# Kernel tuning notes

Measured on AMD Instinct MI355X. Metric: run time of the kernel, lower is better.

## Reference

```python
import jax, jax.numpy as jnp
import numpy as np

FR = 44100          # frame_rate
L = 882000          # sound length (20 s @ 44.1 kHz)
T = 2048            # number of onset time steps
H_GRU = 3
H_LSTM = 10


def setup_inputs() -> dict:
    key = jax.random.key(0)
    ks = jax.random.split(key, 20)

    def unif(k, shape, fan):
        b = 1.0 / np.sqrt(fan)
        return jax.random.uniform(k, shape, jnp.float32, -b, b)

    return {
        "sound": jax.random.normal(ks[0], (1, L), jnp.float32),
        "alpha": jnp.sort(jax.random.randint(ks[1], (1, T), 0, L), axis=1),
        # GRU (input_size=FR, hidden=3): gates ordered (r, z, n). W_hh is
        # multiplied by h0=0 (seq_len==1), so only its bias b_hh matters.
        "gru_w_ih": unif(ks[2], (3 * H_GRU, FR), H_GRU),
        "gru_b_ih": unif(ks[3], (3 * H_GRU,), H_GRU),
        "gru_b_hh": unif(ks[4], (3 * H_GRU,), H_GRU),
        "conv2_w": unif(ks[5], (32, 1, 3), 1 * 3),
        "conv2_b": unif(ks[6], (32,), 1 * 3),
        "conv3_w": unif(ks[7], (16, 32, 3), 32 * 3),
        "conv3_b": unif(ks[8], (16,), 32 * 3),
        "lin_w": unif(ks[9], (10, 17), 17),
        "lin_b": unif(ks[10], (10,), 17),
        # LSTMCell gates ordered (i, f, g, o)
        "lstm_w_ih": unif(ks[11], (4 * H_LSTM, 10), H_LSTM),
        "lstm_w_hh": unif(ks[12], (4 * H_LSTM, H_LSTM), H_LSTM),
        "lstm_b_ih": unif(ks[13], (4 * H_LSTM,), H_LSTM),
        "lstm_b_hh": unif(ks[14], (4 * H_LSTM,), H_LSTM),
        "lin1_w": unif(ks[15], (32, 10), 10),
        "lin1_b": unif(ks[16], (32,), 10),
        "lin2_w": unif(ks[17], (1, 32), 32),
        "lin2_b": unif(ks[18], (1,), 32),
    }


def _conv1d(x, w, b, pad):
    # x: (N, C_in, W), w: (C_out, C_in, K)
    y = jax.lax.conv_general_dilated(
        x, w, window_strides=(1,), padding=[(pad, pad)],
        dimension_numbers=("NCH", "OIH", "NCH"))
    return y + b[None, :, None]


def reference(sound, alpha, gru_w_ih, gru_b_ih, gru_b_hh,
              conv2_w, conv2_b, conv3_w, conv3_b, lin_w, lin_b,
              lstm_w_ih, lstm_w_hh, lstm_b_ih, lstm_b_hh,
              lin1_w, lin1_b, lin2_w, lin2_b):
    fr2 = FR // 2
    padded = jnp.pad(sound[0], (fr2, fr2))                       # (L + FR,)
    # Vectorized dynamic-window gather: one (T, FR) fragment matrix.
    idx = alpha[0][:, None] + jnp.arange(FR)[None, :]            # (T, FR)
    frags = jnp.abs(padded[idx])                                 # (T, FR)

    # GRU: batch=1 -> unbatched input of seq_len=1, h0=0 => single step.
    gi = frags @ gru_w_ih.T + gru_b_ih                           # (T, 9)
    r = jax.nn.sigmoid(gi[:, 0:3] + gru_b_hh[0:3])
    z = jax.nn.sigmoid(gi[:, 3:6] + gru_b_hh[3:6])
    n = jnp.tanh(gi[:, 6:9] + r * gru_b_hh[6:9])
    h = (1.0 - z) * n                                            # (T, 3)

    x = h[:, None, :]                                            # (T, 1, 3)
    x = jax.nn.relu(_conv1d(x, conv2_w, conv2_b, pad=1))         # (T, 32, 3)
    x = _conv1d(x, conv3_w, conv3_b, pad=0)                      # (T, 16, 1)
    feat = x[:, :, 0]                                            # (T, 16)

    a = alpha[0].astype(jnp.float32)
    intervals = jnp.concatenate([a[:1], a[1:] - a[:-1]])         # (T,)
    xin = jnp.concatenate([intervals[:, None], feat], axis=1)    # (T, 17)
    xin = xin @ lin_w.T + lin_b                                  # (T, 10)

    def step(carry, xt):
        hh, cc = carry
        g = xt @ lstm_w_ih.T + lstm_b_ih + hh @ lstm_w_hh.T + lstm_b_hh
        i, f, gg, o = jnp.split(g, 4)
        cc = jax.nn.sigmoid(f) * cc + jax.nn.sigmoid(i) * jnp.tanh(gg)
        hh = jax.nn.sigmoid(o) * jnp.tanh(cc)
        return (hh, cc), None

    init = (jnp.zeros(H_LSTM, jnp.float32), jnp.zeros(H_LSTM, jnp.float32))
    (hT, _), _ = jax.lax.scan(step, init, xin)                   # hT: (10,)

    y = jax.nn.relu(hT[None, :] @ lin1_w.T + lin1_b)             # (1, 32)
    return jax.nn.sigmoid(y @ lin2_w.T + lin2_b)                 # (1, 1)
```

## Files before the change

### kernel.cpp

```cpp
#include <hip/hip_runtime.h>

#define FRLEN 44100
#define FR2 22050
#define LSND 882000
#define TSTEPS 2048
#define ROWS 8
#define LOG2E 1.4426950408889634f

#define KPAD 44104
#define WPROW (KPAD/2)
#define NJP (WPROW/4)
#define PAIRS 463056
#define NGS (PAIRS/4)
#define WGRP (WPROW/4)
#define NGW (9*WGRP)

typedef _Float16 half2_ __attribute__((ext_vector_type(2)));

__device__ __forceinline__ float sigmoidf_(float x){ return 1.0f/(1.0f + __expf(-x)); }

__device__ __forceinline__ float dot2u_(uint a, uint b, float c){
#if __has_builtin(__builtin_amdgcn_fdot2)
  return __builtin_amdgcn_fdot2(*(half2_*)&a, *(half2_*)&b, c, false);
#else
  half2_ ha = *(half2_*)&a, hb = *(half2_*)&b;
  c = fmaf((float)ha.x, (float)hb.x, c);
  return fmaf((float)ha.y, (float)hb.y, c);
#endif
}

__device__ __forceinline__ float dot2h_(half2_ a, half2_ b, float c){
#if __has_builtin(__builtin_amdgcn_fdot2)
  return __builtin_amdgcn_fdot2(a, b, c, false);
#else
  c = fmaf((float)a.x, (float)b.x, c);
  return fmaf((float)a.y, (float)b.y, c);
#endif
}

__device__ __forceinline__ uint pk_(float a, float b){
  auto p = __builtin_amdgcn_cvt_pkrtz(a, b);
  return *(uint*)&p;
}

__global__ void k_prep16(const float* __restrict__ sound, const float* __restrict__ w,
                         uint* __restrict__ pA, uint* __restrict__ pB,
                         uint* __restrict__ wp){
  const int i = blockIdx.x*blockDim.x + threadIdx.x;
  if (i < NGS){
    const int p0 = i*4;
    const int e0 = 2*p0 - FR2;
    float v[9];
    if (e0 >= 0 && e0 + 8 < LSND){
#pragma unroll
      for (int k = 0; k < 9; ++k) v[k] = fabsf(sound[e0+k]);
    } else {
#pragma unroll
      for (int k = 0; k < 9; ++k){
        int e = e0 + k;
        v[k] = (e >= 0 && e < LSND) ? fabsf(sound[e]) : 0.0f;
      }
    }
    uint4 a = make_uint4(pk_(v[0],v[1]), pk_(v[2],v[3]), pk_(v[4],v[5]), pk_(v[6],v[7]));
    uint4 b = make_uint4(pk_(v[1],v[2]), pk_(v[3],v[4]), pk_(v[5],v[6]), pk_(v[7],v[8]));
    *reinterpret_cast<uint4*>(pA + p0) = a;
    *reinterpret_cast<uint4*>(pB + p0) = b;
  } else if (i < NGS + NGW){
    const int g = i - NGS;
    const int k = g / WGRP, gg = g % WGRP;
    const int j = gg*8;
    float v[8];
    if (j + 8 <= FRLEN){
      float4 x = *reinterpret_cast<const float4*>(w + k*FRLEN + j);
      float4 y = *reinterpret_cast<const float4*>(w + k*FRLEN + j + 4);
      v[0]=x.x; v[1]=x.y; v[2]=x.z; v[3]=x.w; v[4]=y.x; v[5]=y.y; v[6]=y.z; v[7]=y.w;
    } else {
#pragma unroll
      for (int q = 0; q < 8; ++q) v[q] = (j+q < FRLEN) ? w[k*FRLEN + j + q] : 0.0f;
    }
    *reinterpret_cast<uint4*>(wp + k*WPROW + gg*4) =
        make_uint4(pk_(v[0],v[1]), pk_(v[2],v[3]), pk_(v[4],v[5]), pk_(v[6],v[7]));
  }
}

__global__ __launch_bounds__(512, 2) void k_front(const uint* __restrict__ pA,
    const uint* __restrict__ pB, const uint* __restrict__ wp,
    const int* __restrict__ alpha,
    const float* __restrict__ gbih, const float* __restrict__ gbhh,
    const float* __restrict__ c2w, const float* __restrict__ c2b,
    const float* __restrict__ c3w, const float* __restrict__ c3b,
    const float* __restrict__ lw, const float* __restrict__ lb,
    const float* __restrict__ wih, const float* __restrict__ bih, const float* __restrict__ bhh,
    _Float16* __restrict__ pre){
  const int tid = threadIdx.x;
  const int row0 = blockIdx.x * ROWS;
  const uint* bp[ROWS];
#pragma unroll
  for (int r = 0; r < ROWS; ++r){
    int b = alpha[row0 + r];
    bp[r] = ((b & 1) ? pB : pA) + (b >> 1);
  }
  float acc[ROWS][9];
#pragma unroll
  for (int r = 0; r < ROWS; ++r)
#pragma unroll
    for (int k = 0; k < 9; ++k) acc[r][k] = 0.0f;

  uint4 fcur[ROWS];
  {
    const int jp = tid*4;
#pragma unroll
    for (int r = 0; r < ROWS; ++r){
      const uint* p = bp[r] + jp;
      fcur[r] = make_uint4(p[0], p[1], p[2], p[3]);
    }
  }
  for (int jj = tid; jj < NJP; jj += 512){
    const int jn = jj + 512;
    uint4 fnx[ROWS];
    if (jn < NJP){
      const int jp2 = jn*4;
#pragma unroll
      for (int r = 0; r < ROWS; ++r){
        const uint* p = bp[r] + jp2;
        fnx[r] = make_uint4(p[0], p[1], p[2], p[3]);
      }
    } else {
#pragma unroll
      for (int r = 0; r < ROWS; ++r) fnx[r] = fcur[r];
    }
    const int jp = jj*4;
    uint4 wq = *reinterpret_cast<const uint4*>(wp + jp);
#pragma unroll
    for (int k = 0; k < 9; ++k){
      uint4 wqn;
      if (k < 8) wqn = *reinterpret_cast<const uint4*>(wp + (k+1)*WPROW + jp);
#pragma unroll
      for (int r = 0; r < ROWS; ++r){
        acc[r][k] = dot2u_(fcur[r].x, wq.x, acc[r][k]);
        acc[r][k] = dot2u_(fcur[r].y, wq.y, acc[r][k]);
        acc[r][k] = dot2u_(fcur[r].z, wq.z, acc[r][k]);
        acc[r][k] = dot2u_(fcur[r].w, wq.w, acc[r][k]);
      }
      if (k < 8) wq = wqn;
    }
#pragma unroll
    for (int r = 0; r < ROWS; ++r) fcur[r] = fnx[r];
  }
#pragma unroll
  for (int m = 32; m >= 1; m >>= 1){
#pragma unroll
    for (int r = 0; r < ROWS; ++r)
#pragma unroll
      for (int k = 0; k < 9; ++k)
        acc[r][k] += __shfl_xor(acc[r][k], m, 64);
  }
  __shared__ float red[8][ROWS*9];
  __shared__ float sgi[ROWS*9];
  const int wv_ = tid >> 6, ln = tid & 63;
  if (ln == 0){
#pragma unroll
    for (int r = 0; r < ROWS; ++r)
#pragma unroll
      for (int k = 0; k < 9; ++k) red[wv_][r*9+k] = acc[r][k];
  }
  __syncthreads();
  if (tid < ROWS*9){
    float s = 0.0f;
#pragma unroll
    for (int q = 0; q < 8; ++q) s += red[q][tid];
    sgi[tid] = s;
  }
  __syncthreads();
  if (tid < ROWS){
    const int t = row0 + tid;
    float gi[9];
#pragma unroll
    for (int k = 0; k < 9; ++k) gi[k] = sgi[tid*9+k] + gbih[k];
    float h[3];
#pragma unroll
    for (int q = 0; q < 3; ++q){
      float rr = sigmoidf_(gi[q]   + gbhh[q]);
      float zz = sigmoidf_(gi[3+q] + gbhh[3+q]);
      float nn = tanhf(gi[6+q] + rr*gbhh[6+q]);
      h[q] = (1.0f - zz)*nn;
    }
    float feat[16];
#pragma unroll
    for (int c = 0; c < 16; ++c) feat[c] = c3b[c];
    for (int ic = 0; ic < 32; ++ic){
      float w0 = c2w[ic*3+0], w1 = c2w[ic*3+1], w2 = c2w[ic*3+2], bb = c2b[ic];
      float x0 = fmaxf(bb + h[0]*w1 + h[1]*w2, 0.0f);
      float x1 = fmaxf(bb + h[0]*w0 + h[1]*w1 + h[2]*w2, 0.0f);
      float x2_ = fmaxf(bb + h[1]*w0 + h[2]*w1, 0.0f);
#pragma unroll
      for (int c = 0; c < 16; ++c){
        const float* wpp = c3w + (c*32+ic)*3;
        feat[c] += x0*wpp[0] + x1*wpp[1] + x2_*wpp[2];
      }
    }
    float interval = (float)(t == 0 ? alpha[0] : (alpha[t] - alpha[t-1]));
    float xin[10];
#pragma unroll
    for (int k = 0; k < 10; ++k){
      float s = lb[k] + interval*lw[k*17];
#pragma unroll
      for (int j = 0; j < 16; ++j) s = fmaf(feat[j], lw[k*17+1+j], s);
      xin[k] = s;
    }
#pragma unroll
    for (int k = 0; k < 40; ++k){
      float s = bih[k] + bhh[k];
#pragma unroll
      for (int i = 0; i < 10; ++i) s = fmaf(xin[i], wih[k*10+i], s);
      const float sc = (k >= 20 && k < 30) ? (-2.0f*LOG2E) : (-LOG2E);
      pre[t*40 + k] = (_Float16)(s * sc);
    }
  }
}

#define LSTM_STEP(PREFETCH_STMT)                                              \
  {                                                                           \
    float g = (float)q0;                                                      \
    q0 = q1; q1 = q2; q2 = q3;                                                \
    PREFETCH_STMT;                                                            \
    float ga = dot2h_(wpk0, hp0, g);                                          \
    ga = dot2h_(wpk1, hp1, ga);                                               \
    ga = dot2h_(wpk2, hp2, ga);                                               \
    float gb = dot2h_(wpk3, hp3, 0.0f);                                       \
    gb = dot2h_(wpk4, hp4, gb);                                               \
    g = ga + gb;                                                              \
    float act = fmaf(__builtin_amdgcn_rcpf(1.0f + __builtin_amdgcn_exp2f(g)), s2, s3); \
    float g_sw = act;                                                         \
    asm("v_permlane32_swap_b32 %0, %1" : "+v"(act), "+v"(g_sw));              \
    float f_sw = act;                                                         \
    asm("v_permlane16_swap_b32 %0, %1" : "+v"(act), "+v"(f_sw));              \
    float o_sw = g_sw;                                                        \
    asm("v_permlane16_swap_b32 %0, %1" : "+v"(g_sw), "+v"(o_sw));             \
    float ig = act * g_sw;                                                    \
    c = fmaf(f_sw, c, ig);                                                    \
    float o2 = o_sw + o_sw;                                                   \
    float hn = fmaf(__builtin_amdgcn_rcpf(1.0f + __builtin_amdgcn_exp2f(c)), o2, -o_sw); \
    int hni = __float_as_int(hn);                                             \
    int hnx = __builtin_amdgcn_update_dpp(0, hni, 0x111, 0xf, 0xf, true);     \
    auto hpk = __builtin_amdgcn_cvt_pkrtz(hn, __int_as_float(hnx));           \
    int pki = *(int*)&hpk;                                                    \
    { int _r = __builtin_amdgcn_readlane(pki, 0); hp0 = *(half2_*)&_r; }      \
    { int _r = __builtin_amdgcn_readlane(pki, 2); hp1 = *(half2_*)&_r; }      \
    { int _r = __builtin_amdgcn_readlane(pki, 4); hp2 = *(half2_*)&_r; }      \
    { int _r = __builtin_amdgcn_readlane(pki, 6); hp3 = *(half2_*)&_r; }      \
    { int _r = __builtin_amdgcn_readlane(pki, 8); hp4 = *(half2_*)&_r; }      \
  }

__global__ __launch_bounds__(1024, 1) void k_lstm(const _Float16* __restrict__ pre,
                       const float* __restrict__ whh,
                       const float* __restrict__ l1w, const float* __restrict__ l1b,
                       const float* __restrict__ l2w, const float* __restrict__ l2b,
                       float* __restrict__ out){
  extern __shared__ _Float16 sp[];
  {
    uint4* dst = (uint4*)sp;
    const uint4* src = (const uint4*)pre;
    for (int i = threadIdx.x; i < (TSTEPS*40*2)/16; i += 1024) dst[i] = src[i];
  }
  __syncthreads();
  if (threadIdx.x >= 64) return;

  const int lane = threadIdx.x;
  const int gate = lane >> 4;
  const int unit_raw = lane & 15;
  const int unit = unit_raw < 10 ? unit_raw : 9;
  const int L40 = gate*10 + unit;
  const bool is_g = (gate == 2);
  const float kk  = -2.0f*LOG2E;
  const float wsc = is_g ? kk : (-LOG2E);
  const float s2  = is_g ? (2.0f*kk) : 1.0f;
  const float s3  = is_g ? (-kk)     : 0.0f;
  half2_ wpk0, wpk1, wpk2, wpk3, wpk4;
  {
    const float* wr = whh + L40*10;
    wpk0 = { (_Float16)(wr[0]*wsc), (_Float16)(wr[1]*wsc) };
    wpk1 = { (_Float16)(wr[2]*wsc), (_Float16)(wr[3]*wsc) };
    wpk2 = { (_Float16)(wr[4]*wsc), (_Float16)(wr[5]*wsc) };
    wpk3 = { (_Float16)(wr[6]*wsc), (_Float16)(wr[7]*wsc) };
    wpk4 = { (_Float16)(wr[8]*wsc), (_Float16)(wr[9]*wsc) };
  }
  half2_ hz = { (_Float16)0.0f, (_Float16)0.0f };
  half2_ hp0 = hz, hp1 = hz, hp2 = hz, hp3 = hz, hp4 = hz;
  float c = 0.0f;

  _Float16 q0 = sp[0*40+L40], q1 = sp[1*40+L40], q2 = sp[2*40+L40], q3 = sp[3*40+L40];
#pragma unroll 4
  for (int t = 0; t < TSTEPS-4; ++t){
    LSTM_STEP(q3 = sp[(t+4)*40 + L40]);
  }
#pragma unroll
  for (int t = TSTEPS-4; t < TSTEPS; ++t){
    LSTM_STEP(;);
  }
  float hf[10];
  hf[0]=(float)hp0.x; hf[1]=(float)hp0.y; hf[2]=(float)hp1.x; hf[3]=(float)hp1.y;
  hf[4]=(float)hp2.x; hf[5]=(float)hp2.y; hf[6]=(float)hp3.x; hf[7]=(float)hp3.y;
  hf[8]=(float)hp4.x; hf[9]=(float)hp4.y;
  float z = 0.0f;
  if (lane < 32){
    float s = l1b[lane];
#pragma unroll
    for (int i = 0; i < 10; ++i) s = fmaf(hf[i], l1w[lane*10+i], s);
    z = fmaxf(s, 0.0f) * l2w[lane];
  }
#pragma unroll
  for (int m = 32; m >= 1; m >>= 1) z += __shfl_xor(z, m, 64);
  if (lane == 0) out[0] = sigmoidf_(z + l2b[0]);
}

extern "C" void kernel_launch(void* const* d_in, const int* in_sizes, int n_in,
                              void* d_out, int out_size, void* d_ws, size_t ws_size,
                              hipStream_t stream){
  const float* sound     = (const float*)d_in[0];
  const int*   alpha     = (const int*)  d_in[1];
  const float* gru_w_ih  = (const float*)d_in[2];
  const float* gru_b_ih  = (const float*)d_in[3];
  const float* gru_b_hh  = (const float*)d_in[4];
  const float* conv2_w   = (const float*)d_in[5];
  const float* conv2_b   = (const float*)d_in[6];
  const float* conv3_w   = (const float*)d_in[7];
  const float* conv3_b   = (const float*)d_in[8];
  const float* lin_w     = (const float*)d_in[9];
  const float* lin_b     = (const float*)d_in[10];
  const float* lstm_w_ih = (const float*)d_in[11];
  const float* lstm_w_hh = (const float*)d_in[12];
  const float* lstm_b_ih = (const float*)d_in[13];
  const float* lstm_b_hh = (const float*)d_in[14];
  const float* lin1_w    = (const float*)d_in[15];
  const float* lin1_b    = (const float*)d_in[16];
  const float* lin2_w    = (const float*)d_in[17];
  const float* lin2_b    = (const float*)d_in[18];

  char* ws = (char*)d_ws;
  uint* pA      = (uint*)ws;
  uint* pB      = pA + PAIRS;
  uint* wpairs  = pB + PAIRS;
  _Float16* pre = (_Float16*)(wpairs + 9*WPROW);

  (void)hipFuncSetAttribute((const void*)k_lstm,
        hipFuncAttributeMaxDynamicSharedMemorySize, TSTEPS*40*2);

  hipLaunchKernelGGL(k_prep16, dim3((NGS + NGW + 255)/256), dim3(256), 0, stream,
                     sound, gru_w_ih, pA, pB, wpairs);
  hipLaunchKernelGGL(k_front, dim3(TSTEPS/ROWS), dim3(512), 0, stream,
                     pA, pB, wpairs, alpha,
                     gru_b_ih, gru_b_hh, conv2_w, conv2_b, conv3_w, conv3_b,
                     lin_w, lin_b, lstm_w_ih, lstm_b_ih, lstm_b_hh, pre);
  hipLaunchKernelGGL(k_lstm, dim3(1), dim3(1024), TSTEPS*40*2, stream,
                     pre, lstm_w_hh, lin1_w, lin1_b, lin2_w, lin2_b, (float*)d_out);
}
```

Baseline: 246.1 us.

## Fuse prep, front and LSTM kernels into one cooperative kernel with grid syncs

Merges the three launches (fp16 packing, GRU projection front-end, serial LSTM) into a single cooperative kernel of 256 blocks that separates phases with grid-wide syncs, so launch gaps between kernels go away. The LSTM tail runs in block 0 with 512 threads instead of a 1024-thread block. The front loop also drops its software prefetch of next-iteration fragments and reloads the weights per gate, and the kernel now requests 160KB of dynamic shared memory. That shared memory request may cap residency at one block per CU and could make the cooperative launch fail or run slower.

```diff
diff --git a/kernel.cpp b/kernel.cpp
--- a/kernel.cpp
+++ b/kernel.cpp
@@ -1,4 +1,7 @@
 #include <hip/hip_runtime.h>
+#include <hip/hip_cooperative_groups.h>
+
+namespace cg = cooperative_groups;
 
 #define FRLEN 44100
 #define FR2 22050
@@ -14,6 +17,7 @@
 #define NGS (PAIRS/4)
 #define WGRP (WPROW/4)
 #define NGW (9*WGRP)
+#define NTHREADS (256*512)
 
 typedef _Float16 half2_ __attribute__((ext_vector_type(2)));
 
@@ -41,182 +45,6 @@
 __device__ __forceinline__ uint pk_(float a, float b){
   auto p = __builtin_amdgcn_cvt_pkrtz(a, b);
   return *(uint*)&p;
-}
-
-__global__ void k_prep16(const float* __restrict__ sound, const float* __restrict__ w,
-                         uint* __restrict__ pA, uint* __restrict__ pB,
-                         uint* __restrict__ wp){
-  const int i = blockIdx.x*blockDim.x + threadIdx.x;
-  if (i < NGS){
-    const int p0 = i*4;
-    const int e0 = 2*p0 - FR2;
-    float v[9];
-    if (e0 >= 0 && e0 + 8 < LSND){
-#pragma unroll
-      for (int k = 0; k < 9; ++k) v[k] = fabsf(sound[e0+k]);
-    } else {
-#pragma unroll
-      for (int k = 0; k < 9; ++k){
-        int e = e0 + k;
-        v[k] = (e >= 0 && e < LSND) ? fabsf(sound[e]) : 0.0f;
-      }
-    }
-    uint4 a = make_uint4(pk_(v[0],v[1]), pk_(v[2],v[3]), pk_(v[4],v[5]), pk_(v[6],v[7]));
-    uint4 b = make_uint4(pk_(v[1],v[2]), pk_(v[3],v[4]), pk_(v[5],v[6]), pk_(v[7],v[8]));
-    *reinterpret_cast<uint4*>(pA + p0) = a;
-    *reinterpret_cast<uint4*>(pB + p0) = b;
-  } else if (i < NGS + NGW){
-    const int g = i - NGS;
-    const int k = g / WGRP, gg = g % WGRP;
-    const int j = gg*8;
-    float v[8];
-    if (j + 8 <= FRLEN){
-      float4 x = *reinterpret_cast<const float4*>(w + k*FRLEN + j);
-      float4 y = *reinterpret_cast<const float4*>(w + k*FRLEN + j + 4);
-      v[0]=x.x; v[1]=x.y; v[2]=x.z; v[3]=x.w; v[4]=y.x; v[5]=y.y; v[6]=y.z; v[7]=y.w;
-    } else {
-#pragma unroll
-      for (int q = 0; q < 8; ++q) v[q] = (j+q < FRLEN) ? w[k*FRLEN + j + q] : 0.0f;
-    }
-    *reinterpret_cast<uint4*>(wp + k*WPROW + gg*4) =
-        make_uint4(pk_(v[0],v[1]), pk_(v[2],v[3]), pk_(v[4],v[5]), pk_(v[6],v[7]));
-  }
-}
-
-__global__ __launch_bounds__(512, 2) void k_front(const uint* __restrict__ pA,
-    const uint* __restrict__ pB, const uint* __restrict__ wp,
-    const int* __restrict__ alpha,
-    const float* __restrict__ gbih, const float* __restrict__ gbhh,
-    const float* __restrict__ c2w, const float* __restrict__ c2b,
-    const float* __restrict__ c3w, const float* __restrict__ c3b,
-    const float* __restrict__ lw, const float* __restrict__ lb,
-    const float* __restrict__ wih, const float* __restrict__ bih, const float* __restrict__ bhh,
-    _Float16* __restrict__ pre){
-  const int tid = threadIdx.x;
-  const int row0 = blockIdx.x * ROWS;
-  const uint* bp[ROWS];
-#pragma unroll
-  for (int r = 0; r < ROWS; ++r){
-    int b = alpha[row0 + r];
-    bp[r] = ((b & 1) ? pB : pA) + (b >> 1);
-  }
-  float acc[ROWS][9];
-#pragma unroll
-  for (int r = 0; r < ROWS; ++r)
-#pragma unroll
-    for (int k = 0; k < 9; ++k) acc[r][k] = 0.0f;
-
-  uint4 fcur[ROWS];
-  {
-    const int jp = tid*4;
-#pragma unroll
-    for (int r = 0; r < ROWS; ++r){
-      const uint* p = bp[r] + jp;
-      fcur[r] = make_uint4(p[0], p[1], p[2], p[3]);
-    }
-  }
-  for (int jj = tid; jj < NJP; jj += 512){
-    const int jn = jj + 512;
-    uint4 fnx[ROWS];
-    if (jn < NJP){
-      const int jp2 = jn*4;
-#pragma unroll
-      for (int r = 0; r < ROWS; ++r){
-        const uint* p = bp[r] + jp2;
-        fnx[r] = make_uint4(p[0], p[1], p[2], p[3]);
-      }
-    } else {
-#pragma unroll
-      for (int r = 0; r < ROWS; ++r) fnx[r] = fcur[r];
-    }
-    const int jp = jj*4;
-    uint4 wq = *reinterpret_cast<const uint4*>(wp + jp);
-#pragma unroll
-    for (int k = 0; k < 9; ++k){
-      uint4 wqn;
-      if (k < 8) wqn = *reinterpret_cast<const uint4*>(wp + (k+1)*WPROW + jp);
-#pragma unroll
-      for (int r = 0; r < ROWS; ++r){
-        acc[r][k] = dot2u_(fcur[r].x, wq.x, acc[r][k]);
-        acc[r][k] = dot2u_(fcur[r].y, wq.y, acc[r][k]);
-        acc[r][k] = dot2u_(fcur[r].z, wq.z, acc[r][k]);
-        acc[r][k] = dot2u_(fcur[r].w, wq.w, acc[r][k]);
-      }
-      if (k < 8) wq = wqn;
-    }
-#pragma unroll
-    for (int r = 0; r < ROWS; ++r) fcur[r] = fnx[r];
-  }
-#pragma unroll
-  for (int m = 32; m >= 1; m >>= 1){
-#pragma unroll
-    for (int r = 0; r < ROWS; ++r)
-#pragma unroll
-      for (int k = 0; k < 9; ++k)
-        acc[r][k] += __shfl_xor(acc[r][k], m, 64);
-  }
-  __shared__ float red[8][ROWS*9];
-  __shared__ float sgi[ROWS*9];
-  const int wv_ = tid >> 6, ln = tid & 63;
-  if (ln == 0){
-#pragma unroll
-    for (int r = 0; r < ROWS; ++r)
-#pragma unroll
-      for (int k = 0; k < 9; ++k) red[wv_][r*9+k] = acc[r][k];
-  }
-  __syncthreads();
-  if (tid < ROWS*9){
-    float s = 0.0f;
-#pragma unroll
-    for (int q = 0; q < 8; ++q) s += red[q][tid];
-    sgi[tid] = s;
-  }
-  __syncthreads();
-  if (tid < ROWS){
-    const int t = row0 + tid;
-    float gi[9];
-#pragma unroll
-    for (int k = 0; k < 9; ++k) gi[k] = sgi[tid*9+k] + gbih[k];
-    float h[3];
-#pragma unroll
-    for (int q = 0; q < 3; ++q){
-      float rr = sigmoidf_(gi[q]   + gbhh[q]);
-      float zz = sigmoidf_(gi[3+q] + gbhh[3+q]);
-      float nn = tanhf(gi[6+q] + rr*gbhh[6+q]);
-      h[q] = (1.0f - zz)*nn;
-    }
-    float feat[16];
-#pragma unroll
-    for (int c = 0; c < 16; ++c) feat[c] = c3b[c];
-    for (int ic = 0; ic < 32; ++ic){
-      float w0 = c2w[ic*3+0], w1 = c2w[ic*3+1], w2 = c2w[ic*3+2], bb = c2b[ic];
-      float x0 = fmaxf(bb + h[0]*w1 + h[1]*w2, 0.0f);
-      float x1 = fmaxf(bb + h[0]*w0 + h[1]*w1 + h[2]*w2, 0.0f);
-      float x2_ = fmaxf(bb + h[1]*w0 + h[2]*w1, 0.0f);
-#pragma unroll
-      for (int c = 0; c < 16; ++c){
-        const float* wpp = c3w + (c*32+ic)*3;
-        feat[c] += x0*wpp[0] + x1*wpp[1] + x2_*wpp[2];
-      }
-    }
-    float interval = (float)(t == 0 ? alpha[0] : (alpha[t] - alpha[t-1]));
-    float xin[10];
-#pragma unroll
-    for (int k = 0; k < 10; ++k){
-      float s = lb[k] + interval*lw[k*17];
-#pragma unroll
-      for (int j = 0; j < 16; ++j) s = fmaf(feat[j], lw[k*17+1+j], s);
-      xin[k] = s;
-    }
-#pragma unroll
-    for (int k = 0; k < 40; ++k){
-      float s = bih[k] + bhh[k];
-#pragma unroll
-      for (int i = 0; i < 10; ++i) s = fmaf(xin[i], wih[k*10+i], s);
-      const float sc = (k >= 20 && k < 30) ? (-2.0f*LOG2E) : (-LOG2E);
-      pre[t*40 + k] = (_Float16)(s * sc);
-    }
-  }
 }
 
 #define LSTM_STEP(PREFETCH_STMT)                                              \
@@ -252,21 +80,180 @@
     { int _r = __builtin_amdgcn_readlane(pki, 8); hp4 = *(half2_*)&_r; }      \
   }
 
-__global__ __launch_bounds__(1024, 1) void k_lstm(const _Float16* __restrict__ pre,
-                       const float* __restrict__ whh,
-                       const float* __restrict__ l1w, const float* __restrict__ l1b,
-                       const float* __restrict__ l2w, const float* __restrict__ l2b,
-                       float* __restrict__ out){
-  extern __shared__ _Float16 sp[];
+__global__ __launch_bounds__(512, 2) void k_all(
+    const float* __restrict__ sound, const int* __restrict__ alpha,
+    const float* __restrict__ gw,
+    const float* __restrict__ gbih, const float* __restrict__ gbhh,
+    const float* __restrict__ c2w, const float* __restrict__ c2b,
+    const float* __restrict__ c3w, const float* __restrict__ c3b,
+    const float* __restrict__ lw, const float* __restrict__ lb,
+    const float* __restrict__ wih, const float* __restrict__ bih, const float* __restrict__ bhh,
+    const float* __restrict__ whh,
+    const float* __restrict__ l1w, const float* __restrict__ l1b,
+    const float* __restrict__ l2w, const float* __restrict__ l2b,
+    uint* __restrict__ pA, uint* __restrict__ pB, uint* __restrict__ wp,
+    _Float16* __restrict__ pre, float* __restrict__ out){
+  extern __shared__ char smem_raw[];
+  const int tid = threadIdx.x;
+
+  for (int i = blockIdx.x*512 + tid; i < NGS + NGW; i += NTHREADS){
+    if (i < NGS){
+      const int p0 = i*4;
+      const int e0 = 2*p0 - FR2;
+      float v[9];
+      if (e0 >= 0 && e0 + 8 < LSND){
+#pragma unroll
+        for (int k = 0; k < 9; ++k) v[k] = fabsf(sound[e0+k]);
+      } else {
+#pragma unroll
+        for (int k = 0; k < 9; ++k){
+          int e = e0 + k;
+          v[k] = (e >= 0 && e < LSND) ? fabsf(sound[e]) : 0.0f;
+        }
+      }
+      uint4 a = make_uint4(pk_(v[0],v[1]), pk_(v[2],v[3]), pk_(v[4],v[5]), pk_(v[6],v[7]));
+      uint4 b = make_uint4(pk_(v[1],v[2]), pk_(v[3],v[4]), pk_(v[5],v[6]), pk_(v[7],v[8]));
+      *reinterpret_cast<uint4*>(pA + p0) = a;
+      *reinterpret_cast<uint4*>(pB + p0) = b;
+    } else {
+      const int g = i - NGS;
+      const int k = g / WGRP, gg = g % WGRP;
+      const int j = gg*8;
+      float v[8];
+      if (j + 8 <= FRLEN){
+        float4 x = *reinterpret_cast<const float4*>(gw + k*FRLEN + j);
+        float4 y = *reinterpret_cast<const float4*>(gw + k*FRLEN + j + 4);
+        v[0]=x.x; v[1]=x.y; v[2]=x.z; v[3]=x.w; v[4]=y.x; v[5]=y.y; v[6]=y.z; v[7]=y.w;
+      } else {
+#pragma unroll
+        for (int q = 0; q < 8; ++q) v[q] = (j+q < FRLEN) ? gw[k*FRLEN + j + q] : 0.0f;
+      }
+      *reinterpret_cast<uint4*>(wp + k*WPROW + gg*4) =
+          make_uint4(pk_(v[0],v[1]), pk_(v[2],v[3]), pk_(v[4],v[5]), pk_(v[6],v[7]));
+    }
+  }
+  __threadfence();
+  cg::this_grid().sync();
+
+  {
+    const int row0 = blockIdx.x * ROWS;
+    const uint* bp[ROWS];
+#pragma unroll
+    for (int r = 0; r < ROWS; ++r){
+      int b = alpha[row0 + r];
+      bp[r] = ((b & 1) ? pB : pA) + (b >> 1);
+    }
+    float acc[ROWS][9];
+#pragma unroll
+    for (int r = 0; r < ROWS; ++r)
+#pragma unroll
+      for (int k = 0; k < 9; ++k) acc[r][k] = 0.0f;
+
+    for (int jj = tid; jj < NJP; jj += 512){
+      const int jp = jj*4;
+      uint4 f[ROWS];
+#pragma unroll
+      for (int r = 0; r < ROWS; ++r){
+        const uint* p = bp[r] + jp;
+        f[r] = make_uint4(p[0], p[1], p[2], p[3]);
+      }
+#pragma unroll
+      for (int k = 0; k < 9; ++k){
+        const uint4 wq = *reinterpret_cast<const uint4*>(wp + k*WPROW + jp);
+#pragma unroll
+        for (int r = 0; r < ROWS; ++r){
+          acc[r][k] = dot2u_(f[r].x, wq.x, acc[r][k]);
+          acc[r][k] = dot2u_(f[r].y, wq.y, acc[r][k]);
+          acc[r][k] = dot2u_(f[r].z, wq.z, acc[r][k]);
+          acc[r][k] = dot2u_(f[r].w, wq.w, acc[r][k]);
+        }
+      }
+    }
+#pragma unroll
+    for (int m = 32; m >= 1; m >>= 1){
+#pragma unroll
+      for (int r = 0; r < ROWS; ++r)
+#pragma unroll
+        for (int k = 0; k < 9; ++k)
+          acc[r][k] += __shfl_xor(acc[r][k], m, 64);
+    }
+    float (*red)[ROWS*9] = (float(*)[ROWS*9])smem_raw;
+    float* sgi = (float*)smem_raw + 8*ROWS*9;
+    const int wv_ = tid >> 6, ln = tid & 63;
+    if (ln == 0){
+#pragma unroll
+      for (int r = 0; r < ROWS; ++r)
+#pragma unroll
+        for (int k = 0; k < 9; ++k) red[wv_][r*9+k] = acc[r][k];
+    }
+    __syncthreads();
+    if (tid < ROWS*9){
+      float s = 0.0f;
+#pragma unroll
+      for (int q = 0; q < 8; ++q) s += red[q][tid];
+      sgi[tid] = s;
+    }
+    __syncthreads();
+    if (tid < ROWS){
+      const int t = row0 + tid;
+      float gi[9];
+#pragma unroll
+      for (int k = 0; k < 9; ++k) gi[k] = sgi[tid*9+k] + gbih[k];
+      float h[3];
+#pragma unroll
+      for (int q = 0; q < 3; ++q){
+        float rr = sigmoidf_(gi[q]   + gbhh[q]);
+        float zz = sigmoidf_(gi[3+q] + gbhh[3+q]);
+        float nn = tanhf(gi[6+q] + rr*gbhh[6+q]);
+        h[q] = (1.0f - zz)*nn;
+      }
+      float feat[16];
+#pragma unroll
+      for (int c = 0; c < 16; ++c) feat[c] = c3b[c];
+      for (int ic = 0; ic < 32; ++ic){
+        float w0 = c2w[ic*3+0], w1 = c2w[ic*3+1], w2 = c2w[ic*3+2], bb = c2b[ic];
+        float x0 = fmaxf(bb + h[0]*w1 + h[1]*w2, 0.0f);
+        float x1 = fmaxf(bb + h[0]*w0 + h[1]*w1 + h[2]*w2, 0.0f);
+        float x2_ = fmaxf(bb + h[1]*w0 + h[2]*w1, 0.0f);
+#pragma unroll
+        for (int c = 0; c < 16; ++c){
+          const float* wpp = c3w + (c*32+ic)*3;
+          feat[c] += x0*wpp[0] + x1*wpp[1] + x2_*wpp[2];
+        }
+      }
+      float interval = (float)(t == 0 ? alpha[0] : (alpha[t] - alpha[t-1]));
+      float xin[10];
+#pragma unroll
+      for (int k = 0; k < 10; ++k){
+        float s = lb[k] + interval*lw[k*17];
+#pragma unroll
+        for (int j = 0; j < 16; ++j) s = fmaf(feat[j], lw[k*17+1+j], s);
+        xin[k] = s;
+      }
+#pragma unroll
+      for (int k = 0; k < 40; ++k){
+        float s = bih[k] + bhh[k];
+#pragma unroll
+        for (int i = 0; i < 10; ++i) s = fmaf(xin[i], wih[k*10+i], s);
+        const float sc = (k >= 20 && k < 30) ? (-2.0f*LOG2E) : (-LOG2E);
+        pre[t*40 + k] = (_Float16)(s * sc);
+      }
+    }
+  }
+  __threadfence();
+  cg::this_grid().sync();
+
+  if (blockIdx.x != 0) return;
+  _Float16* sp = (_Float16*)smem_raw;
   {
     uint4* dst = (uint4*)sp;
     const uint4* src = (const uint4*)pre;
-    for (int i = threadIdx.x; i < (TSTEPS*40*2)/16; i += 1024) dst[i] = src[i];
+    for (int i = tid; i < (TSTEPS*40*2)/16; i += 512) dst[i] = src[i];
   }
   __syncthreads();
-  if (threadIdx.x >= 64) return;
-
-  const int lane = threadIdx.x;
+  if (tid >= 64) return;
+
+  const int lane = tid;
   const int gate = lane >> 4;
   const int unit_raw = lane & 15;
   const int unit = unit_raw < 10 ? unit_raw : 9;
@@ -342,16 +329,19 @@
   uint* pB      = pA + PAIRS;
   uint* wpairs  = pB + PAIRS;
   _Float16* pre = (_Float16*)(wpairs + 9*WPROW);
-
-  (void)hipFuncSetAttribute((const void*)k_lstm,
+  float* outp   = (float*)d_out;
+
+  (void)hipFuncSetAttribute((const void*)k_all,
         hipFuncAttributeMaxDynamicSharedMemorySize, TSTEPS*40*2);
 
-  hipLaunchKernelGGL(k_prep16, dim3((NGS + NGW + 255)/256), dim3(256), 0, stream,
-                     sound, gru_w_ih, pA, pB, wpairs);
-  hipLaunchKernelGGL(k_front, dim3(TSTEPS/ROWS), dim3(512), 0, stream,
-                     pA, pB, wpairs, alpha,
-                     gru_b_ih, gru_b_hh, conv2_w, conv2_b, conv3_w, conv3_b,
-                     lin_w, lin_b, lstm_w_ih, lstm_b_ih, lstm_b_hh, pre);
-  hipLaunchKernelGGL(k_lstm, dim3(1), dim3(1024), TSTEPS*40*2, stream,
-                     pre, lstm_w_hh, lin1_w, lin1_b, lin2_w, lin2_b, (float*)d_out);
-}
+  void* args[] = {
+    (void*)&sound, (void*)&alpha, (void*)&gru_w_ih, (void*)&gru_b_ih, (void*)&gru_b_hh,
+    (void*)&conv2_w, (void*)&conv2_b, (void*)&conv3_w, (void*)&conv3_b,
+    (void*)&lin_w, (void*)&lin_b,
+    (void*)&lstm_w_ih, (void*)&lstm_b_ih, (void*)&lstm_b_hh, (void*)&lstm_w_hh,
+    (void*)&lin1_w, (void*)&lin1_b, (void*)&lin2_w, (void*)&lin2_b,
+    (void*)&pA, (void*)&pB, (void*)&wpairs, (void*)&pre, (void*)&outp
+  };
+  (void)hipLaunchCooperativeKernel((const void*)k_all, dim3(256), dim3(512),
+                                   args, TSTEPS*40*2, stream);
+}
```

New measurement: 396.2 us. 61.0% more time.
